# Kernel optimization log

Measured on AMD Instinct MI355X. Metric: run time of the kernel, lower is better.

## Reference

```python
import jax, jax.numpy as jnp
import numpy as np
from jax import lax

B, T, M = 32, 1024, 40
CONV, H, C = 128, 256, 10
EPS = 1e-5
POOLS = (5, 4, 2)  # mel-axis maxpool sizes; 5*4*2 == n_mels == 40


def setup_inputs() -> dict:
    key = jax.random.key(0)
    ks = jax.random.split(key, 30)
    rn = lambda k, s, sc=0.05: jax.random.normal(k, s, dtype=jnp.float32) * sc
    inp = {}
    inp["features"] = jax.random.normal(ks[0], (B, 1, T, M), dtype=jnp.float32)
    inp["targets"] = (jax.random.uniform(ks[1], (B, T, C)) > 0.5).astype(jnp.float32)
    inp["force_mask"] = jax.random.bernoulli(ks[2], 0.7, (T, B))  # teacher_forcing_prob=0.7
    chans = [(1, CONV), (CONV, CONV), (CONV, CONV)]
    for i, (ci, co) in enumerate(chans, 1):
        inp[f"W{i}"] = rn(ks[3 * i], (co, ci, 5, 5))
        inp[f"b{i}"] = jnp.zeros((co,), jnp.float32)
        inp[f"g{i}"] = jnp.ones((co,), jnp.float32)
        inp[f"be{i}"] = jnp.zeros((co,), jnp.float32)
        inp[f"m{i}"] = rn(ks[3 * i + 1], (co,), 0.01)
        inp[f"v{i}"] = jnp.ones((co,), jnp.float32)
    inp["Wih"] = rn(ks[20], (3 * H, CONV + C))
    inp["Whh"] = rn(ks[21], (3 * H, H))
    inp["bih"] = jnp.zeros((3 * H,), jnp.float32)
    inp["bhh"] = jnp.zeros((3 * H,), jnp.float32)
    inp["Wf"] = rn(ks[22], (C, H))
    inp["bf"] = jnp.zeros((C,), jnp.float32)
    return inp


def _conv_block(x, W, b, g, be, m, v, pool):
    # Conv2d(k=5, s=1, p=2) + BatchNorm2d (inference) + ReLU + MaxPool2d((1,pool))
    y = lax.conv_general_dilated(x, W, window_strides=(1, 1), padding=((2, 2), (2, 2)),
                                 dimension_numbers=("NCHW", "OIHW", "NCHW"))
    y = y + b[None, :, None, None]
    scale = g * lax.rsqrt(v + EPS)
    y = y * scale[None, :, None, None] + (be - m * scale)[None, :, None, None]
    y = jax.nn.relu(y)
    return lax.reduce_window(y, -jnp.inf, lax.max, (1, 1, 1, pool), (1, 1, 1, pool), "VALID")


def _crnn(features, targets, force_mask, W1, b1, g1, be1, m1, v1, W2, b2, g2, be2, m2, v2,
          W3, b3, g3, be3, m3, v3, Wih, Whh, bih, bhh, Wf, bf):
    x = features  # [B,1,T,M]
    for (W, b, g, be, m, v, p) in ((W1, b1, g1, be1, m1, v1, POOLS[0]),
                                   (W2, b2, g2, be2, m2, v2, POOLS[1]),
                                   (W3, b3, g3, be3, m3, v3, POOLS[2])):
        x = _conv_block(x, W, b, g, be, m, v, p)
    feats = jnp.transpose(x[:, :, :, 0], (2, 0, 1))  # mel pooled to 1 -> [T,B,CONV]

    def step(carry, xs):
        h, tf = carry
        xt, tgt_t, ft = xs  # [B,CONV], [B,C], [B]
        inp = jnp.concatenate([xt, tf], axis=-1)  # [B, CONV+C]
        gi = inp @ Wih.T + bih
        gh = h @ Whh.T + bhh
        ir, iz, inn = jnp.split(gi, 3, axis=-1)
        hr, hz, hn = jnp.split(gh, 3, axis=-1)
        r = jax.nn.sigmoid(ir + hr)
        z = jax.nn.sigmoid(iz + hz)
        n = jnp.tanh(inn + r * hn)
        h = (1.0 - z) * n + z * h
        out = h @ Wf.T + bf  # [B,C]
        pred = (jax.nn.sigmoid(out) > 0.5).astype(jnp.float32)
        tf = jnp.where(ft[:, None], tgt_t, pred)  # teacher-forcing select
        return (h, tf), out

    init = (jnp.zeros((B, H), jnp.float32), jnp.zeros((B, C), jnp.float32))
    xs = (feats, jnp.transpose(targets, (1, 0, 2)), force_mask)
    _, outs = lax.scan(step, init, xs)  # [T,B,C]
    return jnp.transpose(outs, (1, 0, 2))  # [B,T,C]


def reference(features, targets, force_mask, W1, b1, g1, be1, m1, v1, W2, b2, g2, be2, m2, v2,
              W3, b3, g3, be3, m3, v3, Wih, Whh, bih, bhh, Wf, bf):
    return _crnn(features, targets, force_mask, W1, b1, g1, be1, m1, v1, W2, b2, g2, be2, m2, v2,
                 W3, b3, g3, be3, m3, v3, Wih, Whh, bih, bhh, Wf, bf)
```

## Files before the change

### kernel.cpp

```cpp
#include <hip/hip_runtime.h>
#include <math.h>

#define EPSF 1e-5f

typedef __attribute__((ext_vector_type(2))) float f2;
typedef __attribute__((ext_vector_type(4))) float f4;
typedef __attribute__((ext_vector_type(8))) _Float16 f16x8;

template<int CTRL>
__device__ __forceinline__ float dpp_add(float v) {
    int s = __builtin_amdgcn_update_dpp(0, __float_as_int(v), CTRL, 0xf, 0xf, true);
    return v + __int_as_float(s);
}

#define HQ(d) ((d) + (((d) >> 4) << 2))

__global__ __launch_bounds__(256) void k_prep(
    const float* __restrict__ Wih, const float* __restrict__ Whh,
    const float* __restrict__ W2, const float* __restrict__ W3,
    const unsigned char* __restrict__ fmask,
    unsigned int* __restrict__ WhhP, float* __restrict__ WxT,
    _Float16* __restrict__ W2F, float* __restrict__ W3T, int* __restrict__ flag)
{
    int idx = blockIdx.x * 256 + threadIdx.x;
    if (idx < 98304) {
        int T = idx >> 8;
        int lane = (idx >> 2) & 63;
        int j = idx & 3;
        int RT = T >> 3, kt = T & 7;
        int row = RT * 16 + (lane & 15);
        int col = kt * 32 + (lane >> 4) * 8 + j * 2;
        union { _Float16 h[2]; unsigned int u; } pk;
        pk.h[0] = (_Float16)Whh[row * 256 + col];
        pk.h[1] = (_Float16)Whh[row * 256 + col + 1];
        WhhP[idx] = pk.u;
    }
    if (idx < 105984) {
        int j = idx / 138, k = idx % 138;
        if (k < 128) WxT[k * 768 + j] = Wih[idx];
    }
    if (idx < 409600) {
        int f = idx & 7, lane = (idx >> 3) & 63, cot = (idx >> 9) & 7;
        int cc = (idx >> 12) & 3, T = idx >> 14;
        int k = cc * 32 + (lane >> 4) * 8 + f;
        int co = cot * 16 + (lane & 15);
        int dt = T / 5, dm = T % 5;
        W2F[idx] = (_Float16)W2[co * 3200 + k * 25 + dt * 5 + dm];
        int co3 = idx / 3200, r = idx % 3200;
        int ci = r / 25, tap = r % 25;
        W3T[(tap * 128 + ci) * 128 + co3] = W3[idx];
    }
    if (idx == 0) {
        int nz = 0;
        for (int i = 0; i < 4096; i++) if ((i & 3) != 0) nz |= fmask[i];
        *flag = nz ? 0 : 1;
    }
}

__global__ __launch_bounds__(256) void k_conv1(
    const float* __restrict__ X, const float* __restrict__ W1,
    const float* __restrict__ bb, const float* __restrict__ gg,
    const float* __restrict__ be, const float* __restrict__ mm_,
    const float* __restrict__ vv, _Float16* __restrict__ X1h,
    _Float16* __restrict__ X1l)
{
    __shared__ __align__(16) float xs[8][44];
    __shared__ __align__(16) float ws[25][128];
    __shared__ float sc[128], sh[128];
    int bid = blockIdx.x;
    int b = bid >> 8, t0 = (bid & 255) << 2;
    int tid = threadIdx.x;
    for (int e = tid; e < 8 * 44; e += 256) {
        int tt = e / 44, mm = e % 44;
        int gt = t0 + tt - 2, gm = mm - 2;
        float val = 0.f;
        if (gt >= 0 && gt < 1024 && gm >= 0 && gm < 40)
            val = X[(b * 1024 + gt) * 40 + gm];
        xs[tt][mm] = val;
    }
    for (int e = tid; e < 3200; e += 256) {
        int tap = e >> 7, co = e & 127;
        ws[tap][co] = W1[co * 25 + tap];
    }
    if (tid < 128) {
        float s = gg[tid] / sqrtf(vv[tid] + EPSF);
        sc[tid] = s;
        sh[tid] = (bb[tid] - mm_[tid]) * s + be[tid];
    }
    __syncthreads();
    int cog = tid >> 5;
    int m1i = (tid >> 2) & 7;
    int tp  = tid & 3;
    int co0 = cog * 16;
    float val[5][16];
#pragma unroll
    for (int p = 0; p < 5; p++)
#pragma unroll
        for (int i = 0; i < 16; i++) val[p][i] = 0.f;
#pragma unroll
    for (int dt = 0; dt < 5; dt++) {
#pragma unroll
        for (int dm = 0; dm < 5; dm++) {
            float w[16];
#pragma unroll
            for (int i = 0; i < 16; i += 4)
                *(float4*)&w[i] = *(const float4*)&ws[dt * 5 + dm][co0 + i];
#pragma unroll
            for (int p = 0; p < 5; p++) {
                float x = xs[tp + dt][m1i * 5 + p + dm];
#pragma unroll
                for (int i = 0; i < 16; i++) val[p][i] = fmaf(x, w[i], val[p][i]);
            }
        }
    }
    f16x8 h0, h1, l0, l1;
#pragma unroll
    for (int i = 0; i < 16; i++) {
        float s = sc[co0 + i], h = sh[co0 + i];
        float mx = 0.f;
#pragma unroll
        for (int p = 0; p < 5; p++) {
            float y = fmaf(val[p][i], s, h);
            y = fmaxf(y, 0.f);
            mx = fmaxf(mx, y);
        }
        _Float16 hh = (_Float16)mx;
        _Float16 ll = (_Float16)(mx - (float)hh);
        if (i < 8) { h0[i] = hh; l0[i] = ll; }
        else       { h1[i - 8] = hh; l1[i - 8] = ll; }
    }
    long off = (((long)(b * 1024 + t0 + tp)) * 8 + m1i) * 128 + co0;
    *(f16x8*)&X1h[off] = h0;
    *(f16x8*)&X1h[off + 8] = h1;
    *(f16x8*)&X1l[off] = l0;
    *(f16x8*)&X1l[off + 8] = l1;
}

__global__ __launch_bounds__(256) void k_conv2(
    const _Float16* __restrict__ X1h, const _Float16* __restrict__ X1l,
    const _Float16* __restrict__ W2F,
    const float* __restrict__ bb, const float* __restrict__ gg,
    const float* __restrict__ be, const float* __restrict__ mm_,
    const float* __restrict__ vv, float* __restrict__ X2)
{
    __shared__ __align__(16) _Float16 xsh[144 * 40];
    __shared__ __align__(16) _Float16 xsl[144 * 40];
    __shared__ float sc[128], sh[128];
    int bid = blockIdx.x;
    int b = bid >> 7, t0 = (bid & 127) << 3;
    int tid = threadIdx.x;
    int wv = tid >> 6, l = tid & 63;
    int rowc = l & 15, ks = (l >> 4) << 3;
    int tloc = rowc >> 3, mloc = rowc & 7;
    if (tid < 128) {
        float s = gg[tid] / sqrtf(vv[tid] + EPSF);
        sc[tid] = s;
        sh[tid] = (bb[tid] - mm_[tid]) * s + be[tid];
    }
    f4 acc[4][2];
#pragma unroll
    for (int Mt = 0; Mt < 4; Mt++) {
        acc[Mt][0] = (f4){0.f, 0.f, 0.f, 0.f};
        acc[Mt][1] = (f4){0.f, 0.f, 0.f, 0.f};
    }

    for (int cc = 0; cc < 4; cc++) {
        __syncthreads();
        for (int e = tid; e < 1152; e += 256) {
            int w2 = (e >= 576) ? 1 : 0;
            int ee = e - 576 * w2;
            int r = ee >> 2, q = ee & 3;
            int tt = r / 12, mm2 = r % 12;
            int gt = t0 + tt - 2, gm = mm2 - 2;
            f16x8 v;
#pragma unroll
            for (int z = 0; z < 8; z++) v[z] = (_Float16)0.f;
            if (gt >= 0 && gt < 1024 && gm >= 0 && gm < 8) {
                const _Float16* src = w2 ? X1l : X1h;
                v = *(const f16x8*)&src[(((long)(b * 1024 + gt)) * 8 + gm) * 128 + cc * 32 + q * 8];
            }
            _Float16* dst = w2 ? xsl : xsh;
            *(f16x8*)&dst[r * 40 + q * 8] = v;
        }
        __syncthreads();
        for (int dt = 0; dt < 5; dt++) {
#pragma unroll
            for (int dm = 0; dm < 5; dm++) {
                const _Float16* wb = &W2F[(((long)((dt * 5 + dm) * 4 + cc) * 8) * 64) * 8];
                f16x8 b0 = *(const f16x8*)&wb[((wv * 2 + 0) * 64 + l) * 8];
                f16x8 b1 = *(const f16x8*)&wb[((wv * 2 + 1) * 64 + l) * 8];
#pragma unroll
                for (int Mt = 0; Mt < 4; Mt++) {
                    int ai = ((Mt * 2 + tloc + dt) * 12 + (mloc + dm)) * 40 + ks;
                    f16x8 ah = *(const f16x8*)&xsh[ai];
                    f16x8 al = *(const f16x8*)&xsl[ai];
                    acc[Mt][0] = __builtin_amdgcn_mfma_f32_16x16x32_f16(ah, b0, acc[Mt][0], 0, 0, 0);
                    acc[Mt][0] = __builtin_amdgcn_mfma_f32_16x16x32_f16(al, b0, acc[Mt][0], 0, 0, 0);
                    acc[Mt][1] = __builtin_amdgcn_mfma_f32_16x16x32_f16(ah, b1, acc[Mt][1], 0, 0, 0);
                    acc[Mt][1] = __builtin_amdgcn_mfma_f32_16x16x32_f16(al, b1, acc[Mt][1], 0, 0, 0);
                }
            }
        }
    }
    int g = l >> 4;
    int tof = g >> 1, m2 = g & 1;
#pragma unroll
    for (int Mt = 0; Mt < 4; Mt++) {
        int t = t0 + Mt * 2 + tof;
#pragma unroll
        for (int c2 = 0; c2 < 2; c2++) {
            int co = (wv * 2 + c2) * 16 + rowc;
            float s = sc[co], h = sh[co];
            f4 av = acc[Mt][c2];
            float mx = 0.f;
#pragma unroll
            for (int j = 0; j < 4; j++) {
                float y = fmaf(av[j], s, h);
                y = fmaxf(y, 0.f);
                mx = fmaxf(mx, y);
            }
            X2[(((long)(b * 1024 + t)) * 2 + m2) * 128 + co] = mx;
        }
    }
}

__global__ __launch_bounds__(256) void k_conv3(
    const float* __restrict__ X2, const float* __restrict__ W3T,
    const float* __restrict__ bb, const float* __restrict__ gg,
    const float* __restrict__ be, const float* __restrict__ mm_,
    const float* __restrict__ vv, float* __restrict__ F)
{
    __shared__ __align__(16) float xs[68 * 66];
    __shared__ __align__(16) float ws[3][32][64];
    __shared__ float sc[64], sh[64];
    int bid = blockIdx.x;
    int coh = bid & 1, t0 = ((bid >> 1) & 15) << 6, b = bid >> 5;
    int co_base = coh * 64;
    int tid = threadIdx.x;
    int tp = tid & 15, cog = tid >> 4;
    if (tid < 64) {
        int co = co_base + tid;
        float s = gg[co] / sqrtf(vv[co] + EPSF);
        sc[tid] = s;
        sh[tid] = (bb[co] - mm_[co]) * s + be[co];
    }
    float acc[4][4][2];
#pragma unroll
    for (int tc = 0; tc < 4; tc++)
#pragma unroll
        for (int c = 0; c < 4; c++) { acc[tc][c][0] = 0.f; acc[tc][c][1] = 0.f; }

    for (int cc = 0; cc < 4; cc++) {
        __syncthreads();
        for (int e = tid; e < 68 * 64; e += 256) {
            int tt = e >> 6, r = e & 63;
            int ci = r >> 1, m = r & 1;
            int gt = t0 + tt - 2;
            float v = 0.f;
            if (gt >= 0 && gt < 1024)
                v = X2[(((long)(b * 1024 + gt)) * 2 + m) * 128 + cc * 32 + ci];
            xs[tt * 66 + ci * 2 + m] = v;
        }
        for (int dt = 0; dt < 5; dt++) {
            __syncthreads();
            for (int e = tid; e < 3 * 32 * 64; e += 256) {
                int co = e & 63, ci = (e >> 6) & 31, dmi = e >> 11;
                ws[dmi][ci][co] = W3T[((dt * 5 + dmi + 1) * 128 + cc * 32 + ci) * 128 + co_base + co];
            }
            __syncthreads();
            for (int ci = 0; ci < 32; ci++) {
                float w1[4], w2[4], w3[4];
                *(float4*)w1 = *(const float4*)&ws[0][ci][cog * 4];
                *(float4*)w2 = *(const float4*)&ws[1][ci][cog * 4];
                *(float4*)w3 = *(const float4*)&ws[2][ci][cog * 4];
#pragma unroll
                for (int tc = 0; tc < 4; tc++) {
                    float2 x = *(const float2*)&xs[(tc * 16 + tp + dt) * 66 + ci * 2];
#pragma unroll
                    for (int c = 0; c < 4; c++) acc[tc][c][0] = fmaf(w2[c], x.x, acc[tc][c][0]);
#pragma unroll
                    for (int c = 0; c < 4; c++) acc[tc][c][0] = fmaf(w3[c], x.y, acc[tc][c][0]);
#pragma unroll
                    for (int c = 0; c < 4; c++) acc[tc][c][1] = fmaf(w1[c], x.x, acc[tc][c][1]);
#pragma unroll
                    for (int c = 0; c < 4; c++) acc[tc][c][1] = fmaf(w2[c], x.y, acc[tc][c][1]);
                }
            }
        }
    }
#pragma unroll
    for (int tc = 0; tc < 4; tc++) {
        float4 ov;
        float* po = (float*)&ov;
#pragma unroll
        for (int c = 0; c < 4; c++) {
            float s = sc[cog * 4 + c], h = sh[cog * 4 + c];
            float y0 = fmaxf(fmaf(acc[tc][c][0], s, h), 0.f);
            float y1 = fmaxf(fmaf(acc[tc][c][1], s, h), 0.f);
            po[c] = fmaxf(y0, y1);
        }
        *(float4*)&F[((long)(t0 + tc * 16 + tp) * 32 + b) * 128 + co_base + cog * 4] = ov;
    }
}

__global__ __launch_bounds__(256) void k_gemm(
    const float* __restrict__ F, const float* __restrict__ WxT,
    const float* __restrict__ bih, const float* __restrict__ bhh,
    float* __restrict__ Gx)
{
    __shared__ __align__(16) float Fs[64][33];
    __shared__ __align__(16) float Ws[32][256];
    int bid = blockIdx.x;
    int jt = bid % 3, tb0 = (bid / 3) * 64;
    int tid = threadIdx.x;
    int tx = tid & 31, ty = tid >> 5;
    float acc[8][8];
#pragma unroll
    for (int i = 0; i < 8; i++)
#pragma unroll
        for (int j = 0; j < 8; j++) acc[i][j] = 0.f;
    for (int cc = 0; cc < 4; cc++) {
        __syncthreads();
        for (int e = tid; e < 64 * 32; e += 256) {
            int ci = e & 31, i = e >> 5;
            Fs[i][ci] = F[(long)(tb0 + i) * 128 + cc * 32 + ci];
        }
        for (int e = tid; e < 32 * 256; e += 256) {
            int jj = e & 255, ci = e >> 8;
            Ws[ci][jj] = WxT[(cc * 32 + ci) * 768 + jt * 256 + jj];
        }
        __syncthreads();
        for (int ci = 0; ci < 32; ci++) {
            float a[8], w[8];
#pragma unroll
            for (int i = 0; i < 8; i++) a[i] = Fs[ty * 8 + i][ci];
            *(float4*)&w[0] = *(const float4*)&Ws[ci][tx * 8];
            *(float4*)&w[4] = *(const float4*)&Ws[ci][tx * 8 + 4];
#pragma unroll
            for (int i = 0; i < 8; i++)
#pragma unroll
                for (int j = 0; j < 8; j++) acc[i][j] = fmaf(a[i], w[j], acc[i][j]);
        }
    }
    float bj[8];
#pragma unroll
    for (int j = 0; j < 8; j++) {
        int col = jt * 256 + tx * 8 + j;
        bj[j] = bih[col] + (col < 512 ? bhh[col] : 0.f);
    }
#pragma unroll
    for (int i = 0; i < 8; i++) {
        float o[8];
#pragma unroll
        for (int j = 0; j < 8; j++) o[j] = acc[i][j] + bj[j];
        float* dst = &Gx[(long)(tb0 + ty * 8 + i) * 768 + jt * 256 + tx * 8];
        *(float4*)&dst[0] = *(float4*)&o[0];
        *(float4*)&dst[4] = *(float4*)&o[4];
    }
}

__global__ __attribute__((amdgpu_waves_per_eu(2, 2))) __launch_bounds__(512) void k_gru2(
    const f16x8* __restrict__ Wp8, const float* __restrict__ Gx,
    const float* __restrict__ Wih, const float* __restrict__ bhh_g,
    const float* __restrict__ Wf, const float* __restrict__ bf_g,
    const float* __restrict__ targets, const unsigned char* __restrict__ fmask,
    const int* __restrict__ flag, float* __restrict__ out)
{
    extern __shared__ __align__(16) _Float16 dynw[];
    __shared__ __align__(16) float hq[320];
    __shared__ __align__(16) _Float16 hqh[256];
    __shared__ __align__(16) _Float16 hqh2[256];
    __shared__ __align__(16) float gsum[768];
    __shared__ float tfl[16];
    __shared__ __align__(16) _Float16 wtfL[7680];
    __shared__ __align__(16) float WfL[3200];
    const int b = blockIdx.x, tid = threadIdx.x;
    const int wv = tid >> 6, l = tid & 63;
    const int kg = l >> 4;
    const int cl = l & 15;
    const bool isGate = (tid < 256);
    const bool isProj = (tid >= 256 && tid < 416);
    const int oc = (tid - 256) >> 4, seg = tid & 15;
    const bool isWr = isProj && (seg == 15);
    f16x8* wlds = (f16x8*)dynw;

    const f16x8* wp = Wp8 + (long)(wv * 48) * 64 + l;

    f16x8 wq[12];
#pragma unroll
    for (int q = 0; q < 12; q++) wq[q] = wp[q * 64];
#pragma unroll
    for (int q = 0; q < 12; q++) asm volatile("" : "+v"(wq[q]));

#pragma unroll
    for (int fi = 0; fi < 15; fi++) wlds[fi * 512 + tid] = wp[(12 + fi) * 64];

    for (int e = tid; e < 7680; e += 512) {
        int cp = e >> 8, jj = e & 255;
        int gg = cp / 10, c = cp - gg * 10;
        wtfL[e] = (_Float16)Wih[(gg * 256 + jj) * 138 + 128 + c];
    }
    for (int e = tid; e < 3200; e += 512) {
        int oo = e / 320, rem = e - oo * 320;
        int sg = rem / 20, ii = rem - sg * 20;
        WfL[e] = (ii < 16) ? Wf[oo * 256 + sg * 16 + ii] : 0.f;
    }
    for (int e = tid; e < 768; e += 512) gsum[e] = 0.f;
    if (tid < 320) hq[tid] = 0.f;
    if (tid < 256) { hqh[tid] = (_Float16)0.f; hqh2[tid] = (_Float16)0.f; }
    if (tid < 16) tfl[tid] = 0.f;
    float bfc = isProj ? bf_g[oc] : 0.f;
    float bh2 = isGate ? bhh_g[tid + 512] : 0.f;
    const int int32mode = flag[0];
    float hold = 0.f;
    const _Float16* bsrc = (cl == 1) ? hqh2 : hqh;
    __syncthreads();

    for (int t = 0; t < 1024; t++) {
        float gxr = 0.f, gxz = 0.f, gxn = 0.f;
        if (isGate) {
            const float* gx = &Gx[((long)t * 32 + b) * 768];
            gxr = gx[tid]; gxz = gx[tid + 256]; gxn = gx[tid + 512];
        }
        float tgt = 0.f; int fmv = 0;
        if (isWr) {
            tgt = targets[((long)b * 1024 + t) * 10 + oc];
            fmv = int32mode ? ((const int*)fmask)[t * 32 + b] : (int)fmask[t * 32 + b];
        }

        f4 acc[6];
#pragma unroll
        for (int rt = 0; rt < 6; rt++) acc[rt] = (f4){0.f, 0.f, 0.f, 0.f};
#pragma unroll
        for (int kt = 0; kt < 8; kt++) {
            f16x8 s4 = wp[(32 + kt) * 64];
            f16x8 s5 = wp[(40 + kt) * 64];
            f16x8 s3;
            if (kt >= 3) s3 = wp[(24 + kt) * 64];
            f16x8 bv = *(const f16x8*)&bsrc[kt * 32 + kg * 8];
            acc[0] = __builtin_amdgcn_mfma_f32_16x16x32_f16(wq[kt], bv, acc[0], 0, 0, 0);
            if (kt < 4)
                acc[1] = __builtin_amdgcn_mfma_f32_16x16x32_f16(wq[8 + kt], bv, acc[1], 0, 0, 0);
            else
                acc[1] = __builtin_amdgcn_mfma_f32_16x16x32_f16(wlds[(kt - 4) * 512 + tid], bv, acc[1], 0, 0, 0);
            acc[2] = __builtin_amdgcn_mfma_f32_16x16x32_f16(wlds[(4 + kt) * 512 + tid], bv, acc[2], 0, 0, 0);
            if (kt < 3)
                acc[3] = __builtin_amdgcn_mfma_f32_16x16x32_f16(wlds[(12 + kt) * 512 + tid], bv, acc[3], 0, 0, 0);
            else
                acc[3] = __builtin_amdgcn_mfma_f32_16x16x32_f16(s3, bv, acc[3], 0, 0, 0);
            acc[4] = __builtin_amdgcn_mfma_f32_16x16x32_f16(s4, bv, acc[4], 0, 0, 0);
            acc[5] = __builtin_amdgcn_mfma_f32_16x16x32_f16(s5, bv, acc[5], 0, 0, 0);
        }
#pragma unroll
        for (int rt = 0; rt < 6; rt++) {
#pragma unroll
            for (int c = 0; c < 4; c++) acc[rt][c] = dpp_add<0x111>(acc[rt][c]);
        }
        if (cl == 1) {
#pragma unroll
            for (int rt = 0; rt < 6; rt++)
                *(f4*)&gsum[(wv * 6 + rt) * 16 + kg * 4] = acc[rt];
        }
        __syncthreads();

        if (isGate) {
            float gr = gxr, gz = gxz, gn = gxn;
#pragma unroll
            for (int c = 0; c < 10; c++) {
                float tv = tfl[c];
                gr = fmaf(tv, (float)wtfL[c * 256 + tid], gr);
                gz = fmaf(tv, (float)wtfL[(10 + c) * 256 + tid], gz);
                gn = fmaf(tv, (float)wtfL[(20 + c) * 256 + tid], gn);
            }
            float ar = gsum[tid];
            float az = gsum[tid + 256];
            float an = gsum[tid + 512] + bh2;
            float r = 1.0f / (1.0f + expf(-(gr + ar)));
            float z = 1.0f / (1.0f + expf(-(gz + az)));
            float n = tanhf(fmaf(r, an, gn));
            float hnew = (1.0f - z) * n + z * hold;
            hold = hnew;
            _Float16 hh = (_Float16)hnew;
            hq[HQ(tid)] = hnew;
            hqh[tid] = hh;
            hqh2[tid] = (_Float16)(hnew - (float)hh);
        }
        __syncthreads();

        if (isProj) {
            float s = 0.f;
#pragma unroll
            for (int qq = 0; qq < 4; qq++) {
                f4 h4 = *(const f4*)&hq[seg * 20 + qq * 4];
                f4 wvv = *(const f4*)&WfL[oc * 320 + seg * 20 + qq * 4];
                s = fmaf(wvv.x, h4.x, s);
                s = fmaf(wvv.y, h4.y, s);
                s = fmaf(wvv.z, h4.z, s);
                s = fmaf(wvv.w, h4.w, s);
            }
            s = dpp_add<0x111>(s);
            s = dpp_add<0x112>(s);
            s = dpp_add<0x114>(s);
            s = dpp_add<0x118>(s);
            if (isWr) {
                float o = s + bfc;
                out[((long)b * 1024 + t) * 10 + oc] = o;
                float pred = (o > 0.f) ? 1.f : 0.f;
                tfl[oc] = fmv ? tgt : pred;
            }
        }
    }
}

extern "C" void kernel_launch(void* const* d_in, const int* in_sizes, int n_in,
                              void* d_out, int out_size, void* d_ws, size_t ws_size,
                              hipStream_t stream) {
    (void)in_sizes; (void)n_in; (void)out_size; (void)ws_size;
    const float* features = (const float*)d_in[0];
    const float* targets  = (const float*)d_in[1];
    const unsigned char* fmask = (const unsigned char*)d_in[2];
    const float* W1  = (const float*)d_in[3];
    const float* b1  = (const float*)d_in[4];
    const float* g1  = (const float*)d_in[5];
    const float* be1 = (const float*)d_in[6];
    const float* m1  = (const float*)d_in[7];
    const float* v1  = (const float*)d_in[8];
    const float* W2  = (const float*)d_in[9];
    const float* b2  = (const float*)d_in[10];
    const float* g2  = (const float*)d_in[11];
    const float* be2 = (const float*)d_in[12];
    const float* m2  = (const float*)d_in[13];
    const float* v2  = (const float*)d_in[14];
    const float* W3  = (const float*)d_in[15];
    const float* b3  = (const float*)d_in[16];
    const float* g3  = (const float*)d_in[17];
    const float* be3 = (const float*)d_in[18];
    const float* m3  = (const float*)d_in[19];
    const float* v3  = (const float*)d_in[20];
    const float* Wih = (const float*)d_in[21];
    const float* Whh = (const float*)d_in[22];
    const float* bih = (const float*)d_in[23];
    const float* bhh = (const float*)d_in[24];
    const float* Wf  = (const float*)d_in[25];
    const float* bf  = (const float*)d_in[26];

    char* w = (char*)d_ws;
    unsigned int* WhhP = (unsigned int*)(w + 0);
    float* WxT = (float*)(w + 786432);
    _Float16* W2F = (_Float16*)(w + 1179648);
    float* W3T = (float*)(w + 2818048);
    int*   flag = (int*)(w + 4456448);
    _Float16* X1h = (_Float16*)(w + 4456960);
    _Float16* X1l = (_Float16*)(w + 4456960 + 67108864);
    float* Gx  = (float*)(w + 4456960);
    float* X2  = (float*)(w + 4456960 + 134217728);
    float* F   = (float*)(w + 4456960 + 134217728 + 33554432);
    float* out = (float*)d_out;

    const int GRU_DYN_LDS = 15 * 512 * 16;
    (void)hipFuncSetAttribute((const void*)k_gru2,
        hipFuncAttributeMaxDynamicSharedMemorySize, GRU_DYN_LDS);

    k_prep<<<1600, 256, 0, stream>>>(Wih, Whh, W2, W3, fmask, WhhP, WxT, W2F, W3T, flag);
    k_conv1<<<8192, 256, 0, stream>>>(features, W1, b1, g1, be1, m1, v1, X1h, X1l);
    k_conv2<<<4096, 256, 0, stream>>>(X1h, X1l, W2F, b2, g2, be2, m2, v2, X2);
    k_conv3<<<1024, 256, 0, stream>>>(X2, W3T, b3, g3, be3, m3, v3, F);
    k_gemm<<<1536, 256, 0, stream>>>(F, WxT, bih, bhh, Gx);
    k_gru2<<<32, 512, GRU_DYN_LDS, stream>>>((const f16x8*)WhhP, Gx, Wih, bhh, Wf, bf,
                                             targets, fmask, flag, out);
}
```

Before: 3.351 ms.

## Move conv3 to split-fp16 MFMA with hi/lo operands

Rewrites the third conv block to use 16x16x32 fp16 MFMA instructions. Activations and weights are each split into fp16 high and low parts, and three MFMAs per tile approximate fp32 accuracy. conv2 now writes its output as fp16 hi/lo pairs, and the prep kernel packs W3 into the MFMA fragment layout. The goal is to replace the scalar FP32 FMA loop that dominates conv3. The cost is more launched blocks with small tiles, per-lane weight loads straight from global memory, and a slight loss of precision.

```diff
diff --git a/kernel.cpp b/kernel.cpp
--- a/kernel.cpp
+++ b/kernel.cpp
@@ -20,7 +20,8 @@
     const float* __restrict__ W2, const float* __restrict__ W3,
     const unsigned char* __restrict__ fmask,
     unsigned int* __restrict__ WhhP, float* __restrict__ WxT,
-    _Float16* __restrict__ W2F, float* __restrict__ W3T, int* __restrict__ flag)
+    _Float16* __restrict__ W2F, _Float16* __restrict__ W3Fh,
+    _Float16* __restrict__ W3Fl, int* __restrict__ flag)
 {
     int idx = blockIdx.x * 256 + threadIdx.x;
     if (idx < 98304) {
@@ -46,9 +47,10 @@
         int co = cot * 16 + (lane & 15);
         int dt = T / 5, dm = T % 5;
         W2F[idx] = (_Float16)W2[co * 3200 + k * 25 + dt * 5 + dm];
-        int co3 = idx / 3200, r = idx % 3200;
-        int ci = r / 25, tap = r % 25;
-        W3T[(tap * 128 + ci) * 128 + co3] = W3[idx];
+        float w3v = W3[co * 3200 + k * 25 + dt * 5 + dm];
+        _Float16 h3 = (_Float16)w3v;
+        W3Fh[idx] = h3;
+        W3Fl[idx] = (_Float16)(w3v - (float)h3);
     }
     if (idx == 0) {
         int nz = 0;
@@ -141,7 +143,8 @@
     const _Float16* __restrict__ W2F,
     const float* __restrict__ bb, const float* __restrict__ gg,
     const float* __restrict__ be, const float* __restrict__ mm_,
-    const float* __restrict__ vv, float* __restrict__ X2)
+    const float* __restrict__ vv, _Float16* __restrict__ X2h,
+    _Float16* __restrict__ X2l)
 {
     __shared__ __align__(16) _Float16 xsh[144 * 40];
     __shared__ __align__(16) _Float16 xsl[144 * 40];
@@ -219,87 +222,96 @@
                 y = fmaxf(y, 0.f);
                 mx = fmaxf(mx, y);
             }
-            X2[(((long)(b * 1024 + t)) * 2 + m2) * 128 + co] = mx;
+            long oi = (((long)(b * 1024 + t)) * 2 + m2) * 128 + co;
+            _Float16 hh = (_Float16)mx;
+            X2h[oi] = hh;
+            X2l[oi] = (_Float16)(mx - (float)hh);
         }
     }
 }
 
 __global__ __launch_bounds__(256) void k_conv3(
-    const float* __restrict__ X2, const float* __restrict__ W3T,
+    const _Float16* __restrict__ X2h, const _Float16* __restrict__ X2l,
+    const _Float16* __restrict__ W3Fh, const _Float16* __restrict__ W3Fl,
     const float* __restrict__ bb, const float* __restrict__ gg,
     const float* __restrict__ be, const float* __restrict__ mm_,
     const float* __restrict__ vv, float* __restrict__ F)
 {
-    __shared__ __align__(16) float xs[68 * 66];
-    __shared__ __align__(16) float ws[3][32][64];
-    __shared__ float sc[64], sh[64];
+    __shared__ __align__(16) _Float16 xsh[24 * 40];
+    __shared__ __align__(16) _Float16 xsl[24 * 40];
+    __shared__ float sc[128], sh[128];
     int bid = blockIdx.x;
-    int coh = bid & 1, t0 = ((bid >> 1) & 15) << 6, b = bid >> 5;
-    int co_base = coh * 64;
+    int b = bid >> 7, t0 = (bid & 127) << 3;
     int tid = threadIdx.x;
-    int tp = tid & 15, cog = tid >> 4;
-    if (tid < 64) {
-        int co = co_base + tid;
-        float s = gg[co] / sqrtf(vv[co] + EPSF);
+    int wv = tid >> 6, l = tid & 63;
+    int rowc = l & 15, ks = (l >> 4) << 3;
+    if (tid < 128) {
+        float s = gg[tid] / sqrtf(vv[tid] + EPSF);
         sc[tid] = s;
-        sh[tid] = (bb[co] - mm_[co]) * s + be[co];
-    }
-    float acc[4][4][2];
-#pragma unroll
-    for (int tc = 0; tc < 4; tc++)
-#pragma unroll
-        for (int c = 0; c < 4; c++) { acc[tc][c][0] = 0.f; acc[tc][c][1] = 0.f; }
+        sh[tid] = (bb[tid] - mm_[tid]) * s + be[tid];
+    }
+    f4 acc[2];
+    acc[0] = (f4){0.f, 0.f, 0.f, 0.f};
+    acc[1] = (f4){0.f, 0.f, 0.f, 0.f};
 
     for (int cc = 0; cc < 4; cc++) {
         __syncthreads();
-        for (int e = tid; e < 68 * 64; e += 256) {
-            int tt = e >> 6, r = e & 63;
-            int ci = r >> 1, m = r & 1;
+        for (int e = tid; e < 192; e += 256) {
+            int w2 = (e >= 96) ? 1 : 0;
+            int r = e - 96 * w2;
+            int row = r >> 2, q = r & 3;
+            int tt = row >> 1, mm2 = row & 1;
             int gt = t0 + tt - 2;
-            float v = 0.f;
-            if (gt >= 0 && gt < 1024)
-                v = X2[(((long)(b * 1024 + gt)) * 2 + m) * 128 + cc * 32 + ci];
-            xs[tt * 66 + ci * 2 + m] = v;
-        }
+            f16x8 v;
+#pragma unroll
+            for (int z = 0; z < 8; z++) v[z] = (_Float16)0.f;
+            if (gt >= 0 && gt < 1024) {
+                const _Float16* src = w2 ? X2l : X2h;
+                v = *(const f16x8*)&src[(((long)(b * 1024 + gt)) * 2 + mm2) * 128 + cc * 32 + q * 8];
+            }
+            _Float16* dst = w2 ? xsl : xsh;
+            *(f16x8*)&dst[row * 40 + q * 8] = v;
+        }
+        __syncthreads();
         for (int dt = 0; dt < 5; dt++) {
-            __syncthreads();
-            for (int e = tid; e < 3 * 32 * 64; e += 256) {
-                int co = e & 63, ci = (e >> 6) & 31, dmi = e >> 11;
-                ws[dmi][ci][co] = W3T[((dt * 5 + dmi + 1) * 128 + cc * 32 + ci) * 128 + co_base + co];
-            }
-            __syncthreads();
-            for (int ci = 0; ci < 32; ci++) {
-                float w1[4], w2[4], w3[4];
-                *(float4*)w1 = *(const float4*)&ws[0][ci][cog * 4];
-                *(float4*)w2 = *(const float4*)&ws[1][ci][cog * 4];
-                *(float4*)w3 = *(const float4*)&ws[2][ci][cog * 4];
-#pragma unroll
-                for (int tc = 0; tc < 4; tc++) {
-                    float2 x = *(const float2*)&xs[(tc * 16 + tp + dt) * 66 + ci * 2];
-#pragma unroll
-                    for (int c = 0; c < 4; c++) acc[tc][c][0] = fmaf(w2[c], x.x, acc[tc][c][0]);
-#pragma unroll
-                    for (int c = 0; c < 4; c++) acc[tc][c][0] = fmaf(w3[c], x.y, acc[tc][c][0]);
-#pragma unroll
-                    for (int c = 0; c < 4; c++) acc[tc][c][1] = fmaf(w1[c], x.x, acc[tc][c][1]);
-#pragma unroll
-                    for (int c = 0; c < 4; c++) acc[tc][c][1] = fmaf(w2[c], x.y, acc[tc][c][1]);
+#pragma unroll
+            for (int dmi = 0; dmi < 3; dmi++) {
+                int dm = dmi + 1;
+                const long wb = (((long)((dt * 5 + dm) * 4 + cc) * 8) * 64) * 8;
+                f16x8 b0h = *(const f16x8*)&W3Fh[wb + ((wv * 2 + 0) * 64 + l) * 8];
+                f16x8 b0l = *(const f16x8*)&W3Fl[wb + ((wv * 2 + 0) * 64 + l) * 8];
+                f16x8 b1h = *(const f16x8*)&W3Fh[wb + ((wv * 2 + 1) * 64 + l) * 8];
+                f16x8 b1l = *(const f16x8*)&W3Fl[wb + ((wv * 2 + 1) * 64 + l) * 8];
+                int mprime = (rowc & 1) + dm - 2;
+                bool valid = (mprime >= 0) && (mprime <= 1);
+                int row = rowc + dt * 2 + dm - 2;
+                int ai = valid ? (row * 40 + ks) : 0;
+                f16x8 ah = *(const f16x8*)&xsh[ai];
+                f16x8 al = *(const f16x8*)&xsl[ai];
+                if (!valid) {
+#pragma unroll
+                    for (int z = 0; z < 8; z++) { ah[z] = (_Float16)0.f; al[z] = (_Float16)0.f; }
                 }
-            }
-        }
-    }
-#pragma unroll
-    for (int tc = 0; tc < 4; tc++) {
-        float4 ov;
-        float* po = (float*)&ov;
-#pragma unroll
-        for (int c = 0; c < 4; c++) {
-            float s = sc[cog * 4 + c], h = sh[cog * 4 + c];
-            float y0 = fmaxf(fmaf(acc[tc][c][0], s, h), 0.f);
-            float y1 = fmaxf(fmaf(acc[tc][c][1], s, h), 0.f);
-            po[c] = fmaxf(y0, y1);
-        }
-        *(float4*)&F[((long)(t0 + tc * 16 + tp) * 32 + b) * 128 + co_base + cog * 4] = ov;
+                acc[0] = __builtin_amdgcn_mfma_f32_16x16x32_f16(ah, b0h, acc[0], 0, 0, 0);
+                acc[0] = __builtin_amdgcn_mfma_f32_16x16x32_f16(ah, b0l, acc[0], 0, 0, 0);
+                acc[0] = __builtin_amdgcn_mfma_f32_16x16x32_f16(al, b0h, acc[0], 0, 0, 0);
+                acc[1] = __builtin_amdgcn_mfma_f32_16x16x32_f16(ah, b1h, acc[1], 0, 0, 0);
+                acc[1] = __builtin_amdgcn_mfma_f32_16x16x32_f16(ah, b1l, acc[1], 0, 0, 0);
+                acc[1] = __builtin_amdgcn_mfma_f32_16x16x32_f16(al, b1h, acc[1], 0, 0, 0);
+            }
+        }
+    }
+    int g = l >> 4;
+#pragma unroll
+    for (int c2 = 0; c2 < 2; c2++) {
+        int co = (wv * 2 + c2) * 16 + rowc;
+        float s = sc[co], h = sh[co];
+#pragma unroll
+        for (int j2 = 0; j2 < 2; j2++) {
+            float y0 = fmaxf(fmaf(acc[c2][j2 * 2], s, h), 0.f);
+            float y1 = fmaxf(fmaf(acc[c2][j2 * 2 + 1], s, h), 0.f);
+            F[((long)(t0 + g * 2 + j2) * 32 + b) * 128 + co] = fmaxf(y0, y1);
+        }
     }
 }
 
@@ -548,12 +560,14 @@
     unsigned int* WhhP = (unsigned int*)(w + 0);
     float* WxT = (float*)(w + 786432);
     _Float16* W2F = (_Float16*)(w + 1179648);
-    float* W3T = (float*)(w + 2818048);
+    _Float16* W3Fh = (_Float16*)(w + 2818048);
+    _Float16* W3Fl = (_Float16*)(w + 3637248);
     int*   flag = (int*)(w + 4456448);
     _Float16* X1h = (_Float16*)(w + 4456960);
     _Float16* X1l = (_Float16*)(w + 4456960 + 67108864);
     float* Gx  = (float*)(w + 4456960);
-    float* X2  = (float*)(w + 4456960 + 134217728);
+    _Float16* X2h = (_Float16*)(w + 4456960 + 134217728);
+    _Float16* X2l = (_Float16*)(w + 4456960 + 134217728 + 16777216);
     float* F   = (float*)(w + 4456960 + 134217728 + 33554432);
     float* out = (float*)d_out;
 
@@ -561,10 +575,10 @@
     (void)hipFuncSetAttribute((const void*)k_gru2,
         hipFuncAttributeMaxDynamicSharedMemorySize, GRU_DYN_LDS);
 
-    k_prep<<<1600, 256, 0, stream>>>(Wih, Whh, W2, W3, fmask, WhhP, WxT, W2F, W3T, flag);
+    k_prep<<<1600, 256, 0, stream>>>(Wih, Whh, W2, W3, fmask, WhhP, WxT, W2F, W3Fh, W3Fl, flag);
     k_conv1<<<8192, 256, 0, stream>>>(features, W1, b1, g1, be1, m1, v1, X1h, X1l);
-    k_conv2<<<4096, 256, 0, stream>>>(X1h, X1l, W2F, b2, g2, be2, m2, v2, X2);
-    k_conv3<<<1024, 256, 0, stream>>>(X2, W3T, b3, g3, be3, m3, v3, F);
+    k_conv2<<<4096, 256, 0, stream>>>(X1h, X1l, W2F, b2, g2, be2, m2, v2, X2h, X2l);
+    k_conv3<<<4096, 256, 0, stream>>>(X2h, X2l, W3Fh, W3Fl, b3, g3, be3, m3, v3, F);
     k_gemm<<<1536, 256, 0, stream>>>(F, WxT, bih, bhh, Gx);
     k_gru2<<<32, 512, GRU_DYN_LDS, stream>>>((const f16x8*)WhhP, Gx, Wih, bhh, Wf, bf,
                                              targets, fmask, flag, out);
```

Result: faster. 3.084 ms (median of 2 runs) (-8.0%).
